# Optimization experiments

Hardware: AMD Instinct MI355X
Metric: run time of the kernel (lower is better)

The kernel has to match this reference:

```python
import jax, jax.numpy as jnp
import numpy as np

S, U, NMEL, T = 32, 10, 40, 120
H, D = 768, 256


def setup_inputs() -> dict:
    key = jax.random.key(0)
    ks = jax.random.split(key, 16)
    def p(k, shape, scale=0.03):
        return jax.random.normal(k, shape, jnp.float32) * scale
    inp = {"mel": jax.random.normal(ks[0], (S, U, 1, NMEL, T), jnp.float32)}
    in_sizes = [NMEL, H, H]
    for l in range(3):
        inp[f"Wih{l}"] = p(ks[1 + 4 * l], (4 * H, in_sizes[l]))
        inp[f"Whh{l}"] = p(ks[2 + 4 * l], (4 * H, H))
        inp[f"bih{l}"] = p(ks[3 + 4 * l], (4 * H,))
        inp[f"bhh{l}"] = p(ks[4 + 4 * l], (4 * H,))
    inp["Wproj"] = p(ks[13], (D, H))
    inp["bproj"] = p(ks[14], (D,))
    inp["loss_w"] = jnp.array([10.0], jnp.float32)
    inp["loss_b"] = jnp.array([-5.0], jnp.float32)
    return inp


def _lstm_layer(x, Wih, Whh, bih, bhh):
    # x: (B, T, In) -> (B, T, H). PyTorch gate order: i, f, g, o.
    B = x.shape[0]
    Hh = Whh.shape[1]
    h0 = jnp.zeros((B, Hh), x.dtype)
    c0 = jnp.zeros((B, Hh), x.dtype)
    bias = bih + bhh
    def step(carry, xt):
        h, c = carry
        gates = xt @ Wih.T + h @ Whh.T + bias  # (B, 4H)
        i, f, g, o = jnp.split(gates, 4, axis=-1)
        c = jax.nn.sigmoid(f) * c + jax.nn.sigmoid(i) * jnp.tanh(g)
        h = jax.nn.sigmoid(o) * jnp.tanh(c)
        return (h, c), h
    _, hs = jax.lax.scan(step, (h0, c0), jnp.swapaxes(x, 0, 1))  # (T, B, H)
    return jnp.swapaxes(hs, 0, 1)


def _ge2e(d3, w, b):
    # d3: (S, U, D) unit-norm d-vectors; w, b: (1,) scalars.
    s, u, _ = d3.shape
    cent = d3.mean(axis=1)  # (S, D) per-speaker centroids
    # leave-one-out positive centroid: (U*cent - self) / (U-1)
    pos_cent = (cent[:, None, :] * u - d3) / (u - 1)  # (S, U, D)
    # cosine sim with eps=1e-6 (F.cosine_similarity clamps norms)
    na = jnp.maximum(jnp.linalg.norm(d3, axis=-1), 1e-6)
    npc = jnp.maximum(jnp.linalg.norm(pos_cent, axis=-1), 1e-6)
    pos_cos = jnp.sum(d3 * pos_cent, axis=-1) / (na * npc)  # (S, U)
    pos_sim = w[0] * pos_cos + b[0]
    # negative sims vs other speakers' centroids (eps=1e-8 default)
    nd = jnp.maximum(jnp.linalg.norm(d3, axis=-1), 1e-8)  # (S, U)
    nc = jnp.maximum(jnp.linalg.norm(cent, axis=-1), 1e-8)  # (S,)
    all_cos = jnp.einsum('sud,kd->suk', d3, cent) / (nd[..., None] * nc[None, None, :])
    jj = jnp.arange(s - 1)
    idx = jj[None, :] + (jj[None, :] >= jnp.arange(s)[:, None])  # (S, S-1), skips own speaker
    neg_cos = jnp.take_along_axis(all_cos, jnp.broadcast_to(idx[:, None, :], (s, u, s - 1)), axis=2)
    neg_sim = w[0] * neg_cos + b[0]
    # softmax GE2E loss: -pos + log sum exp(neg)
    loss = jnp.mean(-pos_sim + jax.scipy.special.logsumexp(neg_sim, axis=2))
    return loss, pos_sim.mean(), neg_sim.mean()


def reference(mel, Wih0, Whh0, bih0, bhh0, Wih1, Whh1, bih1, bhh1,
              Wih2, Whh2, bih2, bhh2, Wproj, bproj, loss_w, loss_b):
    s, u = mel.shape[0], mel.shape[1]
    x = mel.reshape(s * u, mel.shape[3], mel.shape[4])  # (B, 40, T)
    x = jnp.transpose(x, (0, 2, 1))  # (B, T, 40)
    for (Wih, Whh, bih, bhh) in ((Wih0, Whh0, bih0, bhh0),
                                 (Wih1, Whh1, bih1, bhh1),
                                 (Wih2, Whh2, bih2, bhh2)):
        x = _lstm_layer(x, Wih, Whh, bih, bhh)
    h = x[:, -1, :]  # last time step
    dvec = h @ Wproj.T + bproj
    dvec = dvec / jnp.linalg.norm(dvec, axis=1, keepdims=True)
    d3 = dvec.reshape(s, u, -1)
    return _ge2e(d3, loss_w, loss_b)
```

## Files before the change

### kernel.cpp

```cpp
#include <hip/hip_runtime.h>
#include <math.h>

#define S_    32
#define U_    10
#define B_    320
#define T_    120
#define NMEL_ 40
#define H_    768
#define G4_   3072
#define D_    256
#define XP_   64
#define K0_   (XP_ + H_)
#define K12_  (2 * H_)
#define NP_   4

#define NB0   48
#define NB12  96
#define NBLK  (NB0 + 2 * NB12)

#define SMEM_BYTES 159744

typedef _Float16 half8 __attribute__((ext_vector_type(8)));
typedef float floatx4 __attribute__((ext_vector_type(4)));

__device__ __forceinline__ float sigm(float x) {
  return 1.f / (1.f + __expf(-x));
}
__device__ __forceinline__ float tanh_f(float x) {
  x = fminf(15.f, fmaxf(-15.f, x));
  float e = __expf(2.f * x);
  return (e - 1.f) / (e + 1.f);
}

template <int AUX>
__device__ __forceinline__ void dma16(const void* g, void* l) {
  __builtin_amdgcn_global_load_lds(
      (const __attribute__((address_space(1))) unsigned int*)g,
      (__attribute__((address_space(3))) unsigned int*)l, 16, 0, AUX);
}

template <int N>
__device__ __forceinline__ void waitvm() {
  __builtin_amdgcn_s_waitcnt(0x3FF0 | (N & 0xF) | ((N >> 4) << 14));
}


__global__ void prep_x0(const float* __restrict__ mel, _Float16* __restrict__ x0) {
  int idx = blockIdx.x * 256 + threadIdx.x;
  if (idx >= B_ * T_ * XP_) return;
  int k = idx & (XP_ - 1);
  int t = (idx >> 6) % T_;
  int b = idx / (XP_ * T_);
  float v = (k < NMEL_) ? mel[((size_t)b * NMEL_ + k) * T_ + t] : 0.f;
  x0[idx] = (_Float16)v;
}

__global__ void prep_w0(const float* __restrict__ Wih, const float* __restrict__ Whh,
                        _Float16* __restrict__ Wc) {
  int idx = blockIdx.x * 256 + threadIdx.x;
  if (idx >= G4_ * K0_) return;
  int k = idx % K0_;
  int n = idx / K0_;
  float v = 0.f;
  if (k < NMEL_)      v = Wih[(size_t)n * NMEL_ + k];
  else if (k >= XP_)  v = Whh[(size_t)n * H_ + (k - XP_)];
  Wc[idx] = (_Float16)v;
}

__global__ void prep_w12(const float* __restrict__ Wih, const float* __restrict__ Whh,
                         _Float16* __restrict__ Wc) {
  int idx = blockIdx.x * 256 + threadIdx.x;
  if (idx >= G4_ * K12_) return;
  int k = idx % K12_;
  int n = idx / K12_;
  float v = (k < H_) ? Wih[(size_t)n * H_ + k] : Whh[(size_t)n * H_ + (k - H_)];
  Wc[idx] = (_Float16)v;
}

__global__ void prep_bias(const float* __restrict__ bih, const float* __restrict__ bhh,
                          float* __restrict__ bias) {
  int idx = blockIdx.x * 256 + threadIdx.x;
  if (idx < G4_) bias[idx] = bih[idx] + bhh[idx];
}


__device__ __forceinline__ void wait_group(int* fl, int sp, int lp, int lane) {
  if (lp < 0 || lp > 2) return;
  if (sp < lp || sp > lp + T_ - 1) return;
  const int tgt = (lp == 0) ? NB0 : NB12;
  const int base = (sp * 3 + lp) * 96;
  int spin = 0;
  for (;;) {
    int v0 = (lane < tgt)
                 ? __hip_atomic_load(&fl[base + lane], __ATOMIC_RELAXED,
                                     __HIP_MEMORY_SCOPE_AGENT) : 1;
    int v1 = (lane + 64 < tgt)
                 ? __hip_atomic_load(&fl[base + 64 + lane], __ATOMIC_RELAXED,
                                     __HIP_MEMORY_SCOPE_AGENT) : 1;
    if (__all(v0 != 0 && v1 != 0)) break;
    __builtin_amdgcn_s_sleep(1);
    if (++spin > 2000000) break;
  }
}

template <int NT, int NSTG, int NC, int CSPLIT, int AUXX>
__device__ __forceinline__ void gemm_merged(
    const _Float16* __restrict__ lwW, _Float16* __restrict__ lwA,
    const char* __restrict__ srcX, int strideX,
    const char* __restrict__ srcH, int strideH,
    int m0, int lane, floatx4 (&acc)[2][NT],
    int* __restrict__ flags, int sprev, int layer) {
  const int lr = lane & 15, quad = lane >> 4;
  const int rrow = lane >> 2, rq = lane & 3;
  const int rqs = rq ^ ((rrow >> 1) & 3);
  const size_t ox0 = ((size_t)(m0 + rrow) * strideX + rqs * 8) * 2;
  const size_t ox1 = ((size_t)(m0 + 16 + rrow) * strideX + rqs * 8) * 2;
  const size_t oh0 = ((size_t)(m0 + rrow) * strideH + rqs * 8) * 2;
  const size_t oh1 = ((size_t)(m0 + 16 + rrow) * strideH + rqs * 8) * 2;

  auto issue = [&](int c) {
    const int slot = c % NSTG;
    char* ld = (char*)lwA + ((size_t)slot * 320 + m0) * 64;
    if (c < CSPLIT) {
      const char* g = srcX + (size_t)c * 64;
      dma16<AUXX>(g + ox0, ld);
      dma16<AUXX>(g + ox1, ld + 1024);
    } else {
      const char* g = srcH + (size_t)(c - CSPLIT) * 64;
      dma16<17>(g + oh0, ld);
      dma16<17>(g + oh1, ld + 1024);
    }
  };

#pragma unroll
  for (int p = 0; p < NSTG; ++p) issue(p);

  const int asw = (quad ^ ((lr >> 1) & 3)) * 8;

#pragma unroll
  for (int c = 0; c < NC; ++c) {
    const int rem = NC - 1 - c;
    if (rem >= NSTG - 1)      waitvm<2 * (NSTG - 1)>();
    else if (rem == 1)        waitvm<2>();
    else                      waitvm<0>();
    const int slot = c % NSTG;
    const _Float16* aB = lwA + ((size_t)slot * 320 + m0 + lr) * 32 + asw;
    half8 a0 = *(const half8*)(aB);
    half8 a1 = *(const half8*)(aB + 16 * 32);
    half8 bf[NT];
#pragma unroll
    for (int nt = 0; nt < NT; ++nt)
      bf[nt] = *(const half8*)(lwW +
               ((size_t)(c * NT * 16 + nt * 16 + lr) * 32 + asw));
#pragma unroll
    for (int nt = 0; nt < NT; ++nt) {
      acc[0][nt] = __builtin_amdgcn_mfma_f32_16x16x32_f16(a0, bf[nt], acc[0][nt], 0, 0, 0);
      acc[1][nt] = __builtin_amdgcn_mfma_f32_16x16x32_f16(a1, bf[nt], acc[1][nt], 0, 0, 0);
    }
    if (c + NSTG < NC) {
      if (c + NSTG == CSPLIT)
        wait_group(flags, sprev, layer, lane);
      issue(c + NSTG);
    }
  }
}

__global__ __launch_bounds__(640)
void lstm_persist(const _Float16* __restrict__ x0,
                  const _Float16* __restrict__ Wc0, const _Float16* __restrict__ Wc1,
                  const _Float16* __restrict__ Wc2,
                  const float* __restrict__ bias, _Float16* __restrict__ hbuf,
                  int* __restrict__ flags) {
  extern __shared__ _Float16 lw[];
  const int bid = blockIdx.x;

  int layer, tile, units, K;
  const _Float16* Wsrc;
  if (bid < NB0)            { layer = 0; tile = bid;              units = 16; K = K0_;  Wsrc = Wc0; }
  else if (bid < NB0+NB12)  { layer = 1; tile = bid - NB0;        units = 8;  K = K12_; Wsrc = Wc1; }
  else                      { layer = 2; tile = bid - NB0 - NB12; units = 8;  K = K12_; Wsrc = Wc2; }
  const int nrows = units * 4;
  const int j0 = tile * units;
  _Float16* lwA = lw + (size_t)(K / 32) * nrows * 32;

  {
    const int total = (K / 32) * nrows * 4;
    for (int idx = threadIdx.x; idx < total; idx += 640) {
      int c = idx / (nrows * 4);
      int rem = idx % (nrows * 4);
      int r = rem >> 2;
      int q = rem & 3;
      int grow = (r / units) * H_ + j0 + (r % units);
      half8 v = *(const half8*)(Wsrc + (size_t)grow * K + c * 32 + q * 8);
      int qs = q ^ ((r >> 1) & 3);
      *(half8*)(lw + ((size_t)(c * nrows + r) * 32 + qs * 8)) = v;
    }
  }
  __syncthreads();

  const int lane = threadIdx.x & 63;
  const int wv = threadIdx.x >> 6;
  const int lr = lane & 15;
  const int quad = lane >> 4;
  const int m0 = wv * 32;
  const int m1 = wv * 32 + 16;
  const int j = j0 + ((units == 16) ? lr : (lr & 7));

  const float bI = bias[layer * G4_ + 0 * H_ + j];
  const float bF = bias[layer * G4_ + 1 * H_ + j];
  const float bG = bias[layer * G4_ + 2 * H_ + j];
  const float bO = bias[layer * G4_ + 3 * H_ + j];

  float cst[2][4] = {{0.f, 0.f, 0.f, 0.f}, {0.f, 0.f, 0.f, 0.f}};

  for (int t = 0; t < T_; ++t) {
    const int s = layer + t;
    const int pprev = (s - 1) & (NP_ - 1);
    const int pcur = s & (NP_ - 1);
    const _Float16* hown = hbuf + (size_t)(layer * NP_ + pprev) * B_ * H_;
    _Float16* hout = hbuf + (size_t)(layer * NP_ + pcur) * B_ * H_;

    floatx4 acc0[2][4];
    floatx4 acc2[2][2];

    if (layer == 0) {
#pragma unroll
      for (int a = 0; a < 2; ++a)
#pragma unroll
        for (int b = 0; b < 4; ++b) acc0[a][b] = (floatx4){0.f, 0.f, 0.f, 0.f};
      gemm_merged<4, 2, 26, 2, 0>(lw, lwA,
          (const char*)(x0 + (size_t)t * XP_), T_ * XP_,
          (const char*)hown, H_, m0, lane, acc0, flags, s - 1, 0);
    } else {
      wait_group(flags, s - 1, layer - 1, lane);
#pragma unroll
      for (int a = 0; a < 2; ++a)
#pragma unroll
        for (int b = 0; b < 2; ++b) acc2[a][b] = (floatx4){0.f, 0.f, 0.f, 0.f};
      const char* xsrc = (const char*)(hbuf + (size_t)((layer - 1) * NP_ + pprev) * B_ * H_);
      gemm_merged<2, 3, 48, 24, 17>(lw, lwA,
          xsrc, H_, (const char*)hown, H_, m0, lane, acc2, flags, s - 1, layer);
    }

    wait_group(flags, s - 3, layer + 1, lane);

    if (layer == 0) {
#pragma unroll
      for (int mt = 0; mt < 2; ++mt)
#pragma unroll
        for (int r = 0; r < 4; ++r) {
          float iv = acc0[mt][0][r] + bI;
          float fv = acc0[mt][1][r] + bF;
          float gv = acc0[mt][2][r] + bG;
          float ov = acc0[mt][3][r] + bO;
          float cn = sigm(fv) * cst[mt][r] + sigm(iv) * tanh_f(gv);
          cst[mt][r] = cn;
          int m = (mt ? m1 : m0) + quad * 4 + r;
          hout[(size_t)m * H_ + j] = (_Float16)(sigm(ov) * tanh_f(cn));
        }
    } else {
#pragma unroll
      for (int mt = 0; mt < 2; ++mt)
#pragma unroll
        for (int r = 0; r < 4; ++r) {
          float t0 = acc2[mt][0][r], t1 = acc2[mt][1][r];
          float p0 = __shfl_xor(t0, 8, 64);
          float p1 = __shfl_xor(t1, 8, 64);
          bool lo = (lr < 8);
          float iv = (lo ? t0 : p0) + bI;
          float fv = (lo ? p0 : t0) + bF;
          float gv = (lo ? t1 : p1) + bG;
          float ov = (lo ? p1 : t1) + bO;
          float cn = sigm(fv) * cst[mt][r] + sigm(iv) * tanh_f(gv);
          cst[mt][r] = cn;
          if (lo) {
            int m = (mt ? m1 : m0) + quad * 4 + r;
            hout[(size_t)m * H_ + j] = (_Float16)(sigm(ov) * tanh_f(cn));
          }
        }
    }

    __syncthreads();
    if (threadIdx.x == 0)
      __hip_atomic_store(&flags[(s * 3 + layer) * 96 + tile], 1, __ATOMIC_RELEASE,
                         __HIP_MEMORY_SCOPE_AGENT);
  }
}

__global__ void dvec_kernel(const _Float16* __restrict__ hlast, const float* __restrict__ Wproj,
                            const float* __restrict__ bproj, float* __restrict__ d3) {
  const int m = blockIdx.x;
  const int d = threadIdx.x;
  const _Float16* h = hlast + (size_t)m * H_;
  const float* w = Wproj + (size_t)d * H_;
  float acc = bproj[d];
  for (int k = 0; k < H_; k++) acc += (float)h[k] * w[k];
  __shared__ float red[256];
  red[d] = acc * acc;
  __syncthreads();
  for (int off = 128; off > 0; off >>= 1) {
    if (d < off) red[d] += red[d + off];
    __syncthreads();
  }
  float nrm = sqrtf(red[0]);
  d3[(size_t)m * D_ + d] = acc / nrm;
}

__device__ float block_reduce_sum(float x, float* red) {
  const int d = threadIdx.x;
  red[d] = x;
  __syncthreads();
  for (int off = 128; off > 0; off >>= 1) {
    if (d < off) red[d] += red[d + off];
    __syncthreads();
  }
  float r = red[0];
  __syncthreads();
  return r;
}

__global__ void cent_kernel(const float* __restrict__ d3, float* __restrict__ cent,
                            float* __restrict__ ncent) {
  const int sIdx = blockIdx.x;
  const int d = threadIdx.x;
  float acc = 0.f;
  for (int u = 0; u < U_; u++) acc += d3[((size_t)sIdx * U_ + u) * D_ + d];
  acc *= (1.f / U_);
  cent[sIdx * D_ + d] = acc;
  __shared__ float red[256];
  float n2 = block_reduce_sum(acc * acc, red);
  if (d == 0) ncent[sIdx] = fmaxf(sqrtf(n2), 1e-8f);
}

__global__ void ge2e_kernel(const float* __restrict__ d3, const float* __restrict__ cent,
                            const float* __restrict__ ncent, const float* __restrict__ loss_w,
                            const float* __restrict__ loss_b, float* __restrict__ accums) {
  const int p = blockIdx.x;
  const int sIdx = p / U_;
  const int d = threadIdx.x;
  __shared__ float red[256];
  __shared__ float sims[S_];

  const float v = d3[(size_t)p * D_ + d];
  const float cs = cent[sIdx * D_ + d];
  const float pc = (cs * U_ - v) * (1.f / (U_ - 1));

  float nv2 = block_reduce_sum(v * v, red);
  float npc2 = block_reduce_sum(pc * pc, red);
  float dotp = block_reduce_sum(v * pc, red);

  const float w = loss_w[0], b = loss_b[0];
  const float na = fmaxf(sqrtf(nv2), 1e-6f);
  const float npc = fmaxf(sqrtf(npc2), 1e-6f);
  const float pos_sim = w * (dotp / (na * npc)) + b;
  const float nd = fmaxf(sqrtf(nv2), 1e-8f);

  for (int k = 0; k < S_; k++) {
    float dk = block_reduce_sum(v * cent[k * D_ + d], red);
    if (d == 0) sims[k] = w * (dk / (nd * ncent[k])) + b;
  }
  __syncthreads();
  if (d == 0) {
    float mx = -1e30f;
    for (int k = 0; k < S_; k++)
      if (k != sIdx) mx = fmaxf(mx, sims[k]);
    float se = 0.f, sn = 0.f;
    for (int k = 0; k < S_; k++)
      if (k != sIdx) { se += expf(sims[k] - mx); sn += sims[k]; }
    float lse = mx + logf(se);
    atomicAdd(&accums[0], -pos_sim + lse);
    atomicAdd(&accums[1], pos_sim);
    atomicAdd(&accums[2], sn);
  }
}

__global__ void finalize_kernel(const float* __restrict__ accums, float* __restrict__ out) {
  if (threadIdx.x == 0) {
    out[0] = accums[0] / (float)(S_ * U_);
    out[1] = accums[1] / (float)(S_ * U_);
    out[2] = accums[2] / (float)(S_ * U_ * (S_ - 1));
  }
}

extern "C" void kernel_launch(void* const* d_in, const int* in_sizes, int n_in,
                              void* d_out, int out_size, void* d_ws, size_t ws_size,
                              hipStream_t stream) {
  const float* mel = (const float*)d_in[0];
  const float* Wih[3] = {(const float*)d_in[1], (const float*)d_in[5], (const float*)d_in[9]};
  const float* Whh[3] = {(const float*)d_in[2], (const float*)d_in[6], (const float*)d_in[10]};
  const float* bih[3] = {(const float*)d_in[3], (const float*)d_in[7], (const float*)d_in[11]};
  const float* bhh[3] = {(const float*)d_in[4], (const float*)d_in[8], (const float*)d_in[12]};
  const float* Wproj = (const float*)d_in[13];
  const float* bproj = (const float*)d_in[14];
  const float* loss_w = (const float*)d_in[15];
  const float* loss_b = (const float*)d_in[16];
  float* out = (float*)d_out;

  char* ws = (char*)d_ws;
  size_t off = 0;
  auto alloc = [&](size_t bytes) -> void* {
    void* p = ws + off;
    off = (off + bytes + 255) & ~(size_t)255;
    return p;
  };
  _Float16* x0   = (_Float16*)alloc((size_t)B_ * T_ * XP_ * 2);
  _Float16* Wc0  = (_Float16*)alloc((size_t)G4_ * K0_ * 2);
  _Float16* Wc1  = (_Float16*)alloc((size_t)G4_ * K12_ * 2);
  _Float16* Wc2  = (_Float16*)alloc((size_t)G4_ * K12_ * 2);
  float*    bias = (float*)alloc((size_t)3 * G4_ * 4);
  _Float16* hbuf = (_Float16*)alloc((size_t)3 * NP_ * B_ * H_ * 2);
  float*    d3   = (float*)alloc((size_t)B_ * D_ * 4);
  float*    cent = (float*)alloc((size_t)S_ * D_ * 4);
  float*    ncent = (float*)alloc((size_t)S_ * 4);
  float*    accums = (float*)alloc(64);
  int*      flags = (int*)alloc((size_t)(T_ + 3) * 3 * 96 * 4);

  hipMemsetAsync(hbuf, 0, (size_t)3 * NP_ * B_ * H_ * 2, stream);
  hipMemsetAsync(accums, 0, 64, stream);
  hipMemsetAsync(flags, 0, (size_t)(T_ + 3) * 3 * 96 * 4, stream);

  prep_x0<<<(B_ * T_ * XP_ + 255) / 256, 256, 0, stream>>>(mel, x0);
  prep_w0<<<(G4_ * K0_ + 255) / 256, 256, 0, stream>>>(Wih[0], Whh[0], Wc0);
  prep_w12<<<(G4_ * K12_ + 255) / 256, 256, 0, stream>>>(Wih[1], Whh[1], Wc1);
  prep_w12<<<(G4_ * K12_ + 255) / 256, 256, 0, stream>>>(Wih[2], Whh[2], Wc2);
  for (int l = 0; l < 3; l++)
    prep_bias<<<(G4_ + 255) / 256, 256, 0, stream>>>(bih[l], bhh[l], bias + l * G4_);

  hipFuncSetAttribute((const void*)lstm_persist,
                      hipFuncAttributeMaxDynamicSharedMemorySize, SMEM_BYTES);
  void* kargs[] = {(void*)&x0, (void*)&Wc0, (void*)&Wc1, (void*)&Wc2,
                   (void*)&bias, (void*)&hbuf, (void*)&flags};
  hipLaunchCooperativeKernel((const void*)lstm_persist, dim3(NBLK), dim3(640),
                             kargs, SMEM_BYTES, stream);

  const _Float16* hlast = hbuf + (size_t)(2 * NP_ + 1) * B_ * H_;
  dvec_kernel<<<B_, 256, 0, stream>>>(hlast, Wproj, bproj, d3);
  cent_kernel<<<S_, 256, 0, stream>>>(d3, cent, ncent);
  ge2e_kernel<<<B_, 256, 0, stream>>>(d3, cent, ncent, loss_w, loss_b, accums);
  finalize_kernel<<<1, 64, 0, stream>>>(accums, out);
}
```

Before: 3.637 ms.

## Add per-XCC leader acquire fence and relax h-state load cache policy

Each block reads its XCC id, and per step the first block on each XCC performs a single agent-scope acquire fence and publishes a per-XCC flag that other blocks on that XCC spin on. The h-state and layer-input DMA loads switch their cache-policy aux bits from 17 to 1, so they rely on the leader's fence for L2 coherence instead of bypassing caches on every load. The aim is cheaper recurrent-state reads through cache. The cost is an extra per-step spin barrier per XCC, and correctness depends on the per-XCC fence making the other blocks' writes visible.

```diff
diff --git a/kernel.cpp b/kernel.cpp
--- a/kernel.cpp
+++ b/kernel.cpp
@@ -103,7 +103,7 @@
   }
 }
 
-template <int NT, int NSTG, int NC, int CSPLIT, int AUXX>
+template <int NT, int NSTG, int NC, int CSPLIT, int AUXX, int AUXH>
 __device__ __forceinline__ void gemm_merged(
     const _Float16* __restrict__ lwW, _Float16* __restrict__ lwA,
     const char* __restrict__ srcX, int strideX,
@@ -127,8 +127,8 @@
       dma16<AUXX>(g + ox1, ld + 1024);
     } else {
       const char* g = srcH + (size_t)(c - CSPLIT) * 64;
-      dma16<17>(g + oh0, ld);
-      dma16<17>(g + oh1, ld + 1024);
+      dma16<AUXH>(g + oh0, ld);
+      dma16<AUXH>(g + oh1, ld + 1024);
     }
   };
 
@@ -170,7 +170,8 @@
                   const _Float16* __restrict__ Wc0, const _Float16* __restrict__ Wc1,
                   const _Float16* __restrict__ Wc2,
                   const float* __restrict__ bias, _Float16* __restrict__ hbuf,
-                  int* __restrict__ flags) {
+                  int* __restrict__ flags, int* __restrict__ tick,
+                  int* __restrict__ leadDone) {
   extern __shared__ _Float16 lw[];
   const int bid = blockIdx.x;
 
@@ -182,6 +183,10 @@
   const int nrows = units * 4;
   const int j0 = tile * units;
   _Float16* lwA = lw + (size_t)(K / 32) * nrows * 32;
+
+  unsigned xcc;
+  asm volatile("s_getreg_b32 %0, hwreg(HW_REG_XCC_ID)" : "=s"(xcc));
+  xcc &= 7;
 
   {
     const int total = (K / 32) * nrows * 4;
@@ -220,6 +225,23 @@
     const _Float16* hown = hbuf + (size_t)(layer * NP_ + pprev) * B_ * H_;
     _Float16* hout = hbuf + (size_t)(layer * NP_ + pcur) * B_ * H_;
 
+    if (threadIdx.x == 0) {
+      if (__hip_atomic_fetch_add(&tick[xcc * 128 + s], 1, __ATOMIC_RELAXED,
+                                 __HIP_MEMORY_SCOPE_AGENT) == 0) {
+        __builtin_amdgcn_fence(__ATOMIC_ACQUIRE, "agent");
+        __hip_atomic_store(&leadDone[xcc * 128 + s], 1, __ATOMIC_RELEASE,
+                           __HIP_MEMORY_SCOPE_AGENT);
+      }
+    }
+    if (lane == 0) {
+      int spin = 0;
+      while (__hip_atomic_load(&leadDone[xcc * 128 + s], __ATOMIC_RELAXED,
+                               __HIP_MEMORY_SCOPE_AGENT) == 0) {
+        __builtin_amdgcn_s_sleep(1);
+        if (++spin > 2000000) break;
+      }
+    }
+
     floatx4 acc0[2][4];
     floatx4 acc2[2][2];
 
@@ -228,7 +250,7 @@
       for (int a = 0; a < 2; ++a)
 #pragma unroll
         for (int b = 0; b < 4; ++b) acc0[a][b] = (floatx4){0.f, 0.f, 0.f, 0.f};
-      gemm_merged<4, 2, 26, 2, 0>(lw, lwA,
+      gemm_merged<4, 2, 26, 2, 0, 1>(lw, lwA,
           (const char*)(x0 + (size_t)t * XP_), T_ * XP_,
           (const char*)hown, H_, m0, lane, acc0, flags, s - 1, 0);
     } else {
@@ -238,7 +260,7 @@
 #pragma unroll
         for (int b = 0; b < 2; ++b) acc2[a][b] = (floatx4){0.f, 0.f, 0.f, 0.f};
       const char* xsrc = (const char*)(hbuf + (size_t)((layer - 1) * NP_ + pprev) * B_ * H_);
-      gemm_merged<2, 3, 48, 24, 17>(lw, lwA,
+      gemm_merged<2, 3, 48, 24, 1, 1>(lw, lwA,
           xsrc, H_, (const char*)hown, H_, m0, lane, acc2, flags, s - 1, layer);
     }
 
@@ -414,10 +436,14 @@
   float*    ncent = (float*)alloc((size_t)S_ * 4);
   float*    accums = (float*)alloc(64);
   int*      flags = (int*)alloc((size_t)(T_ + 3) * 3 * 96 * 4);
+  int*      tick  = (int*)alloc((size_t)8 * 128 * 4);
+  int*      lead  = (int*)alloc((size_t)8 * 128 * 4);
 
   hipMemsetAsync(hbuf, 0, (size_t)3 * NP_ * B_ * H_ * 2, stream);
   hipMemsetAsync(accums, 0, 64, stream);
   hipMemsetAsync(flags, 0, (size_t)(T_ + 3) * 3 * 96 * 4, stream);
+  hipMemsetAsync(tick, 0, (size_t)8 * 128 * 4, stream);
+  hipMemsetAsync(lead, 0, (size_t)8 * 128 * 4, stream);
 
   prep_x0<<<(B_ * T_ * XP_ + 255) / 256, 256, 0, stream>>>(mel, x0);
   prep_w0<<<(G4_ * K0_ + 255) / 256, 256, 0, stream>>>(Wih[0], Whh[0], Wc0);
@@ -429,7 +455,8 @@
   hipFuncSetAttribute((const void*)lstm_persist,
                       hipFuncAttributeMaxDynamicSharedMemorySize, SMEM_BYTES);
   void* kargs[] = {(void*)&x0, (void*)&Wc0, (void*)&Wc1, (void*)&Wc2,
-                   (void*)&bias, (void*)&hbuf, (void*)&flags};
+                   (void*)&bias, (void*)&hbuf, (void*)&flags, (void*)&tick,
+                   (void*)&lead};
   hipLaunchCooperativeKernel((const void*)lstm_persist, dim3(NBLK), dim3(640),
                              kargs, SMEM_BYTES, stream);
 
```

Result: faster. 3.331 ms (-8.4%).
